# Optimization experiments

Hardware: AMD Instinct MI355X
Metric: run time of the kernel (lower is better)

## Reference

```python
import jax, jax.numpy as jnp
import numpy as np

D = 256        # d_model
B = 16
T = 8192
K = 100        # num_anchors
EPS = 1e-12    # normalize eps (matches torch sqrt(sum+eps))
LN_EPS = 1e-5  # nn.LayerNorm default
NEG = float(np.finfo(np.float32).min)


def _p(key, shape, scale=0.02):
    return (jax.random.normal(key, shape, dtype=jnp.float32) * scale)


def setup_inputs() -> dict:
    key = jax.random.key(0)
    ks = jax.random.split(key, 12)
    return {
        "vision_tokens": jax.random.normal(ks[0], (B, T, D), dtype=jnp.float32),
        "text_emb": jax.random.normal(ks[1], (B, D), dtype=jnp.float32),
        # fuse: Linear(2D->D), GELU, Linear(D->D)
        "fuse_w1": _p(ks[2], (2 * D, D)), "fuse_b1": jnp.zeros((D,), jnp.float32),
        "fuse_w2": _p(ks[3], (D, D)),     "fuse_b2": jnp.zeros((D,), jnp.float32),
        # box head: LN, Linear(D->D), GELU, Linear(D->4)
        "box_ln_g": jnp.ones((D,), jnp.float32), "box_ln_b": jnp.zeros((D,), jnp.float32),
        "box_w1": _p(ks[4], (D, D)), "box_b1": jnp.zeros((D,), jnp.float32),
        "box_w2": _p(ks[5], (D, 4)), "box_b2": jnp.zeros((4,), jnp.float32),
        # obj head: LN, Linear(D->D), GELU, Linear(D->1)
        "obj_ln_g": jnp.ones((D,), jnp.float32), "obj_ln_b": jnp.zeros((D,), jnp.float32),
        "obj_w1": _p(ks[6], (D, D)), "obj_b1": jnp.zeros((D,), jnp.float32),
        "obj_w2": _p(ks[7], (D, 1)), "obj_b2": jnp.zeros((1,), jnp.float32),
    }


def _layer_norm(x, g, b):
    mu = jnp.mean(x, axis=-1, keepdims=True)
    var = jnp.mean(jnp.square(x - mu), axis=-1, keepdims=True)
    return (x - mu) * jax.lax.rsqrt(var + LN_EPS) * g + b


def _gelu(x):
    return jax.nn.gelu(x, approximate=False)  # torch nn.GELU default is exact erf


def reference(vision_tokens, text_emb,
              fuse_w1, fuse_b1, fuse_w2, fuse_b2,
              box_ln_g, box_ln_b, box_w1, box_b1, box_w2, box_b2,
              obj_ln_g, obj_ln_b, obj_w1, obj_b1, obj_w2, obj_b2):
    # L2-normalize text embedding (sqrt(sum+eps) variant)
    txt = text_emb / jnp.sqrt(jnp.sum(text_emb * text_emb, axis=-1, keepdims=True) + EPS)  # (B,D)
    # broadcast-concat text to every token and fuse
    txt_b = jnp.broadcast_to(txt[:, None, :], vision_tokens.shape)  # (B,T,D)
    cat = jnp.concatenate([vision_tokens, txt_b], axis=-1)          # (B,T,2D)
    h = _gelu(cat @ fuse_w1 + fuse_b1) @ fuse_w2 + fuse_b2          # (B,T,D)
    # box head -> sigmoid xywh
    bh = _layer_norm(h, box_ln_g, box_ln_b)
    boxes = jax.nn.sigmoid(_gelu(bh @ box_w1 + box_b1) @ box_w2 + box_b2)  # (B,T,4)
    # objectness head -> sigmoid score per token
    oh = _layer_norm(h, obj_ln_g, obj_ln_b)
    obj = jax.nn.sigmoid(_gelu(oh @ obj_w1 + obj_b1) @ obj_w2 + obj_b2)[..., 0]  # (B,T)
    # pad with -inf-like min so topk always has K candidates, then clamp idx to T-1
    pad = jnp.full((obj.shape[0], K), NEG, dtype=obj.dtype)
    obj_pad = jnp.concatenate([obj, pad], axis=1)                   # (B,T+K)
    scores, idx_raw = jax.lax.top_k(obj_pad, K)                     # (B,K)
    idx = jnp.minimum(idx_raw, obj.shape[1] - 1)                    # (B,K)
    top_boxes = jnp.take_along_axis(boxes, idx[..., None], axis=1)  # (B,K,4)
    # cosine similarity of fused tokens vs. text
    tok_n = h / jnp.sqrt(jnp.sum(h * h, axis=-1, keepdims=True) + EPS)
    text_scores_full = jnp.sum(tok_n * txt[:, None, :], axis=-1)    # (B,T)
    top_text_scores = jnp.take_along_axis(text_scores_full, idx, axis=1)  # (B,K)
    return (top_boxes, scores, top_text_scores)
```

## Files before the change

### kernel.cpp

```cpp
#include <hip/hip_runtime.h>
#include <math.h>

#define D 256
#define PD 260
#define TOK_B 16
#define TOK_T 8192
#define NTOK (TOK_B * TOK_T)
#define KSEL 100

typedef unsigned long long ull;

__device__ float g_txt[TOK_B * D];
__device__ float g_obj[NTOK];
__device__ int   g_sel[TOK_B * KSEL];

template <typename F>
__device__ __forceinline__ float np_sum128_f(F f, int base) {
#pragma clang fp contract(off)
  float r0 = f(base + 0), r1 = f(base + 1), r2 = f(base + 2), r3 = f(base + 3);
  float r4 = f(base + 4), r5 = f(base + 5), r6 = f(base + 6), r7 = f(base + 7);
  for (int i = 8; i < 128; i += 8) {
    r0 += f(base + i + 0); r1 += f(base + i + 1);
    r2 += f(base + i + 2); r3 += f(base + i + 3);
    r4 += f(base + i + 4); r5 += f(base + i + 5);
    r6 += f(base + i + 6); r7 += f(base + i + 7);
  }
  return ((r0 + r1) + (r2 + r3)) + ((r4 + r5) + (r6 + r7));
}
template <typename F>
__device__ __forceinline__ float np_sum256_f(F f) {
#pragma clang fp contract(off)
  return np_sum128_f(f, 0) + np_sum128_f(f, 128);
}

template <typename F>
__device__ __forceinline__ float np_sum256_par8(F f, int j) {
#pragma clang fp contract(off)
  float s0 = f(j);
  for (int i = 1; i < 16; ++i) s0 += f(8 * i + j);
  float s1 = f(128 + j);
  for (int i = 1; i < 16; ++i) s1 += f(128 + 8 * i + j);
  s0 += __shfl_xor(s0, 1);
  s0 += __shfl_xor(s0, 2);
  s0 += __shfl_xor(s0, 4);
  s1 += __shfl_xor(s1, 1);
  s1 += __shfl_xor(s1, 2);
  s1 += __shfl_xor(s1, 4);
  return s0 + s1;
}

__device__ __forceinline__ float np_geluf(float x) {
#pragma clang fp contract(off)
  const float t = x / 1.41421356237309504880f;
  const float e = (float)erf((double)t);
  return (0.5f * x) * (1.0f + e);
}
__device__ __forceinline__ float np_sigmoidf(float x) {
#pragma clang fp contract(off)
  return 1.0f / (1.0f + expf(-x));
}

__global__ __launch_bounds__(256) void k0_txt(const float* __restrict__ text_emb) {
#pragma clang fp contract(off)
  const int b = blockIdx.x, tid = threadIdx.x;
  __shared__ float sSq[D];
  __shared__ float sTot;
  const float e = text_emb[b * D + tid];
  sSq[tid] = e * e;
  __syncthreads();
  if (tid == 0) {
    const float* p = sSq;
    sTot = np_sum256_f([&](int i) { return p[i]; });
  }
  __syncthreads();
  g_txt[b * D + tid] = e / sqrtf(sTot + 1e-12f);
}

__device__ __forceinline__ void gemm_acc(const float (*__restrict__ S)[PD],
                                         const float* __restrict__ W, int r0,
                                         int c0, float acc[4][8]) {
  for (int k = 0; k < D; k += 4) {
    float4 A0 = *(const float4*)&S[r0 + 0][k];
    float4 A1 = *(const float4*)&S[r0 + 1][k];
    float4 A2 = *(const float4*)&S[r0 + 2][k];
    float4 A3 = *(const float4*)&S[r0 + 3][k];
    const float ar[4][4] = {{A0.x, A0.y, A0.z, A0.w},
                            {A1.x, A1.y, A1.z, A1.w},
                            {A2.x, A2.y, A2.z, A2.w},
                            {A3.x, A3.y, A3.z, A3.w}};
#pragma unroll
    for (int kk = 0; kk < 4; ++kk) {
      const float* wr = W + (size_t)(k + kk) * D + c0;
      float4 W0 = *(const float4*)wr;
      float4 W1 = *(const float4*)(wr + 4);
      const float wv[8] = {W0.x, W0.y, W0.z, W0.w, W1.x, W1.y, W1.z, W1.w};
#pragma unroll
      for (int i = 0; i < 4; ++i)
#pragma unroll
        for (int j = 0; j < 8; ++j)
          acc[i][j] = fmaf(ar[i][kk], wv[j], acc[i][j]);
    }
  }
}

__global__ __launch_bounds__(256) void k1_obj(
    const float* __restrict__ vision, const float* __restrict__ fuse_w1,
    const float* __restrict__ fuse_b1, const float* __restrict__ fuse_w2,
    const float* __restrict__ fuse_b2, const float* __restrict__ obj_ln_g,
    const float* __restrict__ obj_ln_b, const float* __restrict__ obj_w1,
    const float* __restrict__ obj_b1, const float* __restrict__ obj_w2,
    const float* __restrict__ obj_b2) {
#pragma clang fp contract(off)
  const int tid = threadIdx.x;
  const int tr = tid >> 5, tc = tid & 31;
  const int r0 = tr << 2, c0 = tc << 3;
  const int blk = blockIdx.x;
  const int batch = blk >> 8;

  __shared__ float sA[32][PD];
  __shared__ float sTxt[D];
  __shared__ float sMu[32], sRstd[32];

  {
    const float* src = vision + (size_t)blk * (32 * D);
#pragma unroll
    for (int i = 0; i < 8; ++i) {
      const int e = i * 1024 + tid * 4;
      const int row = e >> 8, col = e & 255;
      *(float4*)&sA[row][col] = *(const float4*)(src + e);
    }
    sTxt[tid] = g_txt[batch * D + tid];
  }
  __syncthreads();

  float acc[4][8];
#pragma unroll
  for (int i = 0; i < 4; ++i)
#pragma unroll
    for (int j = 0; j < 8; ++j) acc[i][j] = 0.0f;

  gemm_acc(sA, fuse_w1, r0, c0, acc);
  for (int k = 0; k < D; ++k) {
    const float tv = sTxt[k];
    const float* wr = fuse_w1 + (size_t)(D + k) * D + c0;
    float4 W0 = *(const float4*)wr;
    float4 W1 = *(const float4*)(wr + 4);
    const float wv[8] = {W0.x, W0.y, W0.z, W0.w, W1.x, W1.y, W1.z, W1.w};
#pragma unroll
    for (int i = 0; i < 4; ++i)
#pragma unroll
      for (int j = 0; j < 8; ++j) acc[i][j] = fmaf(tv, wv[j], acc[i][j]);
  }
  __syncthreads();
  {
#pragma unroll
    for (int j2 = 0; j2 < 8; ++j2) {
      const float b = fuse_b1[c0 + j2];
#pragma unroll
      for (int i = 0; i < 4; ++i)
        sA[r0 + i][c0 + j2] = np_geluf(acc[i][j2] + b);
    }
  }
  __syncthreads();

#pragma unroll
  for (int i = 0; i < 4; ++i)
#pragma unroll
    for (int j = 0; j < 8; ++j) acc[i][j] = 0.0f;
  gemm_acc(sA, fuse_w2, r0, c0, acc);
  __syncthreads();
  {
#pragma unroll
    for (int j2 = 0; j2 < 8; ++j2) {
      const float b = fuse_b2[c0 + j2];
#pragma unroll
      for (int i = 0; i < 4; ++i) sA[r0 + i][c0 + j2] = acc[i][j2] + b;
    }
  }
  __syncthreads();

  {
    const int r = tid >> 3, j = tid & 7;
    const float* hrow = &sA[r][0];
    const float mu =
        np_sum256_par8([&](int i) { return hrow[i]; }, j) / 256.0f;
    const float var = np_sum256_par8(
                          [&](int i) {
                            const float d = hrow[i] - mu;
                            return d * d;
                          },
                          j) /
                      256.0f;
    if (j == 0) {
      sMu[r] = mu;
      sRstd[r] = 1.0f / sqrtf(var + 1e-5f);
    }
  }
  __syncthreads();

  {
    const float lg = obj_ln_g[tid], lb = obj_ln_b[tid];
    for (int r = 0; r < 32; ++r) {
      const float t = (sA[r][tid] - sMu[r]) * sRstd[r];
      sA[r][tid] = t * lg + lb;
    }
  }
  __syncthreads();

#pragma unroll
  for (int i = 0; i < 4; ++i)
#pragma unroll
    for (int j = 0; j < 8; ++j) acc[i][j] = 0.0f;
  gemm_acc(sA, obj_w1, r0, c0, acc);
  __syncthreads();
  {
#pragma unroll
    for (int j2 = 0; j2 < 8; ++j2) {
      const float b = obj_b1[c0 + j2];
#pragma unroll
      for (int i = 0; i < 4; ++i)
        sA[r0 + i][c0 + j2] = np_geluf(acc[i][j2] + b);
    }
  }
  __syncthreads();

  if ((tid & 7) == 0) {
    const int row = tid >> 3;
    const float* q = &sA[row][0];
    float L = 0.0f;
    for (int k = 0; k < D; ++k) L = fmaf(q[k], obj_w2[k], L);
    L = L + obj_b2[0];
    g_obj[(size_t)blk * 32 + row] = np_sigmoidf(L);
  }
}

__global__ __launch_bounds__(256) void k2_topk(float* __restrict__ out_scores) {
  const int b = blockIdx.x, tid = threadIdx.x;
  __shared__ ull sKey[TOK_T];
  __shared__ ull sGmax[128];
  __shared__ int sWin;
  for (int i = tid; i < TOK_T; i += 256) {
    const float s = g_obj[b * TOK_T + i];
    sKey[i] = ((ull)__float_as_uint(s) << 32) | (unsigned)(TOK_T - 1 - i);
  }
  __syncthreads();
  if (tid < 128) {
    ull m = 0ull;
    for (int j = 0; j < 64; ++j) {
      const ull v = sKey[tid + 128 * j];
      m = v > m ? v : m;
    }
    sGmax[tid] = m;
  }
  __syncthreads();
  for (int r = 0; r < KSEL; ++r) {
    if (tid < 64) {
      ull m = sGmax[tid];
      const ull o = sGmax[64 + tid];
      if (o > m) m = o;
#pragma unroll
      for (int off = 32; off > 0; off >>= 1) {
        const ull o2 = __shfl_down(m, off, 64);
        if (o2 > m) m = o2;
      }
      if (tid == 0) {
        const int idx = (TOK_T - 1) - (int)(unsigned)(m & 0xFFFFFFFFull);
        out_scores[b * KSEL + r] = __uint_as_float((unsigned)(m >> 32));
        g_sel[b * KSEL + r] = idx;
        sKey[idx] = 0ull;
        sWin = idx & 127;
      }
    }
    __syncthreads();
    if (tid < 64) {
      const int g = sWin;
      ull v = sKey[g + 128 * tid];
#pragma unroll
      for (int off = 32; off > 0; off >>= 1) {
        const ull o = __shfl_down(v, off, 64);
        if (o > v) v = o;
      }
      if (tid == 0) sGmax[g] = v;
    }
    __syncthreads();
  }
}

__global__ __launch_bounds__(256) void k3_box(
    const float* __restrict__ vision, const float* __restrict__ fuse_w1,
    const float* __restrict__ fuse_b1, const float* __restrict__ fuse_w2,
    const float* __restrict__ fuse_b2, const float* __restrict__ box_ln_g,
    const float* __restrict__ box_ln_b, const float* __restrict__ box_w1,
    const float* __restrict__ box_b1, const float* __restrict__ box_w2,
    const float* __restrict__ box_b2, float* __restrict__ out) {
#pragma clang fp contract(off)
  const int tid = threadIdx.x, c = tid;
  __shared__ float sV[8][PD];
  __shared__ float sG[8][PD];
  __shared__ float sH[8][PD];
  __shared__ float sTx[8][PD];
  __shared__ float sMu[8], sRstd[8];
  __shared__ int sIdx[8], sBat[8];
  if (tid < 8) {
    const int e = blockIdx.x * 8 + tid;
    sBat[tid] = e / KSEL;
    sIdx[tid] = g_sel[e];
  }
  __syncthreads();
  {
    const int u = tid >> 5, col = (tid & 31) * 8;
    const float* src = vision + ((size_t)sBat[u] * TOK_T + sIdx[u]) * D + col;
    *(float4*)&sV[u][col] = *(const float4*)src;
    *(float4*)&sV[u][col + 4] = *(const float4*)(src + 4);
    const float* tsrc = &g_txt[sBat[u] * D + col];
    *(float4*)&sTx[u][col] = *(const float4*)tsrc;
    *(float4*)&sTx[u][col + 4] = *(const float4*)(tsrc + 4);
  }
  __syncthreads();

  float acc[8];
#pragma unroll
  for (int u = 0; u < 8; ++u) acc[u] = 0.0f;
  for (int k = 0; k < D; ++k) {
    const float w = fuse_w1[k * D + c];
#pragma unroll
    for (int u = 0; u < 8; ++u) acc[u] = fmaf(sV[u][k], w, acc[u]);
  }
  for (int k = 0; k < D; ++k) {
    const float w = fuse_w1[(D + k) * D + c];
#pragma unroll
    for (int u = 0; u < 8; ++u) acc[u] = fmaf(sTx[u][k], w, acc[u]);
  }
  {
    const float b = fuse_b1[c];
#pragma unroll
    for (int u = 0; u < 8; ++u) sG[u][c] = np_geluf(acc[u] + b);
  }
  __syncthreads();

#pragma unroll
  for (int u = 0; u < 8; ++u) acc[u] = 0.0f;
  for (int k = 0; k < D; ++k) {
    const float w = fuse_w2[k * D + c];
#pragma unroll
    for (int u = 0; u < 8; ++u) acc[u] = fmaf(sG[u][k], w, acc[u]);
  }
  {
    const float b = fuse_b2[c];
#pragma unroll
    for (int u = 0; u < 8; ++u) sH[u][c] = acc[u] + b;
  }
  __syncthreads();

  {
    const int u = tid >> 3, j = tid & 7;
    if (u < 8) {
      const float* h = &sH[u][0];
      const float* tx = &sTx[u][0];
      const float mu = np_sum256_par8([&](int i) { return h[i]; }, j) / 256.0f;
      const float var = np_sum256_par8(
                            [&](int i) {
                              const float d = h[i] - mu;
                              return d * d;
                            },
                            j) /
                        256.0f;
      const float q2 = np_sum256_par8([&](int i) { return h[i] * h[i]; }, j);
      const float den = sqrtf(q2 + 1e-12f);
      const float ts =
          np_sum256_par8([&](int i) { return (h[i] / den) * tx[i]; }, j);
      if (j == 0) {
        sMu[u] = mu;
        sRstd[u] = 1.0f / sqrtf(var + 1e-5f);
        out[8000 + blockIdx.x * 8 + u] = ts;
      }
    }
  }
  __syncthreads();

  {
    const float lg = box_ln_g[c], lb = box_ln_b[c];
#pragma unroll
    for (int u = 0; u < 8; ++u) {
      const float t = (sH[u][c] - sMu[u]) * sRstd[u];
      sG[u][c] = t * lg + lb;
    }
  }
  __syncthreads();

#pragma unroll
  for (int u = 0; u < 8; ++u) acc[u] = 0.0f;
  for (int k = 0; k < D; ++k) {
    const float w = box_w1[k * D + c];
#pragma unroll
    for (int u = 0; u < 8; ++u) acc[u] = fmaf(sG[u][k], w, acc[u]);
  }
  {
    const float b = box_b1[c];
#pragma unroll
    for (int u = 0; u < 8; ++u) sV[u][c] = np_geluf(acc[u] + b);
  }
  __syncthreads();

  if (tid < 32) {
    const int u = tid >> 2, j = tid & 3;
    const float* q = &sV[u][0];
    float L = 0.0f;
    for (int k = 0; k < D; ++k) L = fmaf(q[k], box_w2[k * 4 + j], L);
    L = L + box_b2[j];
    out[(blockIdx.x * 8 + u) * 4 + j] = np_sigmoidf(L);
  }
}

extern "C" void kernel_launch(void* const* d_in, const int* in_sizes, int n_in,
                              void* d_out, int out_size, void* d_ws,
                              size_t ws_size, hipStream_t stream) {
  const float* vision   = (const float*)d_in[0];
  const float* text_emb = (const float*)d_in[1];
  const float* fuse_w1  = (const float*)d_in[2];
  const float* fuse_b1  = (const float*)d_in[3];
  const float* fuse_w2  = (const float*)d_in[4];
  const float* fuse_b2  = (const float*)d_in[5];
  const float* box_ln_g = (const float*)d_in[6];
  const float* box_ln_b = (const float*)d_in[7];
  const float* box_w1   = (const float*)d_in[8];
  const float* box_b1   = (const float*)d_in[9];
  const float* box_w2   = (const float*)d_in[10];
  const float* box_b2   = (const float*)d_in[11];
  const float* obj_ln_g = (const float*)d_in[12];
  const float* obj_ln_b = (const float*)d_in[13];
  const float* obj_w1   = (const float*)d_in[14];
  const float* obj_b1   = (const float*)d_in[15];
  const float* obj_w2   = (const float*)d_in[16];
  const float* obj_b2   = (const float*)d_in[17];
  float* out = (float*)d_out;

  k0_txt<<<TOK_B, 256, 0, stream>>>(text_emb);
  k1_obj<<<NTOK / 32, 256, 0, stream>>>(
      vision, fuse_w1, fuse_b1, fuse_w2, fuse_b2, obj_ln_g, obj_ln_b, obj_w1,
      obj_b1, obj_w2, obj_b2);
  k2_topk<<<TOK_B, 256, 0, stream>>>(out + 6400);
  k3_box<<<(TOK_B * KSEL) / 8, 256, 0, stream>>>(
      vision, fuse_w1, fuse_b1, fuse_w2, fuse_b2, box_ln_g, box_ln_b, box_w1,
      box_b1, box_w2, box_b2, out);
}
```

Before: 1.404 ms.

## Stage weight tiles through LDS in k1_obj GEMMs instead of direct global loads

The weight matrices in the fused obj-path kernel are now loaded cooperatively into a shared-memory tile of 32 k-rows per step, with a padded per-column-group layout. Each thread then reads its 8 output columns from LDS rather than issuing per-thread global float4 loads. Some barriers are folded into the tile loop, and launch bounds now request 2 blocks per SM. The aim is to cut redundant global/L2 weight traffic; the cost is extra LDS use (about 33 KB more per block), which may reduce occupancy, plus many more barriers.

```diff
diff --git a/kernel.cpp b/kernel.cpp
--- a/kernel.cpp
+++ b/kernel.cpp
@@ -3,10 +3,12 @@
 
 #define D 256
 #define PD 260
+#define SWS 260
 #define TOK_B 16
 #define TOK_T 8192
 #define NTOK (TOK_B * TOK_T)
 #define KSEL 100
+#define ROWS 32
 
 typedef unsigned long long ull;
 
@@ -76,34 +78,86 @@
   g_txt[b * D + tid] = e / sqrtf(sTot + 1e-12f);
 }
 
-__device__ __forceinline__ void gemm_acc(const float (*__restrict__ S)[PD],
-                                         const float* __restrict__ W, int r0,
-                                         int c0, float acc[4][8]) {
-  for (int k = 0; k < D; k += 4) {
-    float4 A0 = *(const float4*)&S[r0 + 0][k];
-    float4 A1 = *(const float4*)&S[r0 + 1][k];
-    float4 A2 = *(const float4*)&S[r0 + 2][k];
-    float4 A3 = *(const float4*)&S[r0 + 3][k];
-    const float ar[4][4] = {{A0.x, A0.y, A0.z, A0.w},
-                            {A1.x, A1.y, A1.z, A1.w},
-                            {A2.x, A2.y, A2.z, A2.w},
-                            {A3.x, A3.y, A3.z, A3.w}};
-#pragma unroll
-    for (int kk = 0; kk < 4; ++kk) {
-      const float* wr = W + (size_t)(k + kk) * D + c0;
-      float4 W0 = *(const float4*)wr;
-      float4 W1 = *(const float4*)(wr + 4);
+__device__ __forceinline__ void gemm_lds(const float (*__restrict__ S)[PD],
+                                         const float* __restrict__ W,
+                                         float* __restrict__ sW, int r0,
+                                         int tc, float acc[4][8]) {
+  const int t = threadIdx.x;
+  const int sg = t & 31, kb = t >> 5;
+  for (int kt = 0; kt < 8; ++kt) {
+    __syncthreads();
+#pragma unroll
+    for (int m = 0; m < 4; ++m) {
+      const int k = kb * 4 + m;
+      const float* src = W + (size_t)(kt * 32 + k) * D + sg * 8;
+      const float4 a = *(const float4*)src;
+      const float4 b = *(const float4*)(src + 4);
+      float* dst = sW + sg * SWS + k * 8;
+      *(float4*)dst = a;
+      *(float4*)(dst + 4) = b;
+    }
+    __syncthreads();
+    const float* wp = sW + tc * SWS;
+    const int kbase = kt * 32;
+    for (int k4 = 0; k4 < 32; k4 += 4) {
+      const float4 A0 = *(const float4*)&S[r0 + 0][kbase + k4];
+      const float4 A1 = *(const float4*)&S[r0 + 1][kbase + k4];
+      const float4 A2 = *(const float4*)&S[r0 + 2][kbase + k4];
+      const float4 A3 = *(const float4*)&S[r0 + 3][kbase + k4];
+      const float ar[4][4] = {{A0.x, A0.y, A0.z, A0.w},
+                              {A1.x, A1.y, A1.z, A1.w},
+                              {A2.x, A2.y, A2.z, A2.w},
+                              {A3.x, A3.y, A3.z, A3.w}};
+#pragma unroll
+      for (int kk = 0; kk < 4; ++kk) {
+        const float4 W0 = *(const float4*)(wp + (k4 + kk) * 8);
+        const float4 W1 = *(const float4*)(wp + (k4 + kk) * 8 + 4);
+        const float wv[8] = {W0.x, W0.y, W0.z, W0.w, W1.x, W1.y, W1.z, W1.w};
+#pragma unroll
+        for (int i = 0; i < 4; ++i)
+#pragma unroll
+          for (int j = 0; j < 8; ++j)
+            acc[i][j] = fmaf(ar[i][kk], wv[j], acc[i][j]);
+      }
+    }
+  }
+}
+
+__device__ __forceinline__ void gemm_txt_lds(const float* __restrict__ sTxt,
+                                             const float* __restrict__ W,
+                                             float* __restrict__ sW, int tc,
+                                             float acc[4][8]) {
+  const int t = threadIdx.x;
+  const int sg = t & 31, kb = t >> 5;
+  for (int kt = 0; kt < 8; ++kt) {
+    __syncthreads();
+#pragma unroll
+    for (int m = 0; m < 4; ++m) {
+      const int k = kb * 4 + m;
+      const float* src = W + (size_t)(kt * 32 + k) * D + sg * 8;
+      const float4 a = *(const float4*)src;
+      const float4 b = *(const float4*)(src + 4);
+      float* dst = sW + sg * SWS + k * 8;
+      *(float4*)dst = a;
+      *(float4*)(dst + 4) = b;
+    }
+    __syncthreads();
+    const float* wp = sW + tc * SWS;
+    const int kbase = kt * 32;
+    for (int k = 0; k < 32; ++k) {
+      const float tv = sTxt[kbase + k];
+      const float4 W0 = *(const float4*)(wp + k * 8);
+      const float4 W1 = *(const float4*)(wp + k * 8 + 4);
       const float wv[8] = {W0.x, W0.y, W0.z, W0.w, W1.x, W1.y, W1.z, W1.w};
 #pragma unroll
       for (int i = 0; i < 4; ++i)
 #pragma unroll
-        for (int j = 0; j < 8; ++j)
-          acc[i][j] = fmaf(ar[i][kk], wv[j], acc[i][j]);
-    }
-  }
-}
-
-__global__ __launch_bounds__(256) void k1_obj(
+        for (int j = 0; j < 8; ++j) acc[i][j] = fmaf(tv, wv[j], acc[i][j]);
+    }
+  }
+}
+
+__global__ __launch_bounds__(256, 2) void k1_obj(
     const float* __restrict__ vision, const float* __restrict__ fuse_w1,
     const float* __restrict__ fuse_b1, const float* __restrict__ fuse_w2,
     const float* __restrict__ fuse_b2, const float* __restrict__ obj_ln_g,
@@ -117,12 +171,13 @@
   const int blk = blockIdx.x;
   const int batch = blk >> 8;
 
-  __shared__ float sA[32][PD];
+  __shared__ float sA[ROWS][PD];
+  __shared__ float sW[32 * SWS];
   __shared__ float sTxt[D];
-  __shared__ float sMu[32], sRstd[32];
-
-  {
-    const float* src = vision + (size_t)blk * (32 * D);
+  __shared__ float sMu[ROWS], sRstd[ROWS];
+
+  {
+    const float* src = vision + (size_t)blk * (ROWS * D);
 #pragma unroll
     for (int i = 0; i < 8; ++i) {
       const int e = i * 1024 + tid * 4;
@@ -131,7 +186,6 @@
     }
     sTxt[tid] = g_txt[batch * D + tid];
   }
-  __syncthreads();
 
   float acc[4][8];
 #pragma unroll
@@ -139,18 +193,8 @@
 #pragma unroll
     for (int j = 0; j < 8; ++j) acc[i][j] = 0.0f;
 
-  gemm_acc(sA, fuse_w1, r0, c0, acc);
-  for (int k = 0; k < D; ++k) {
-    const float tv = sTxt[k];
-    const float* wr = fuse_w1 + (size_t)(D + k) * D + c0;
-    float4 W0 = *(const float4*)wr;
-    float4 W1 = *(const float4*)(wr + 4);
-    const float wv[8] = {W0.x, W0.y, W0.z, W0.w, W1.x, W1.y, W1.z, W1.w};
-#pragma unroll
-    for (int i = 0; i < 4; ++i)
-#pragma unroll
-      for (int j = 0; j < 8; ++j) acc[i][j] = fmaf(tv, wv[j], acc[i][j]);
-  }
+  gemm_lds(sA, fuse_w1, sW, r0, tc, acc);
+  gemm_txt_lds(sTxt, fuse_w1 + (size_t)D * D, sW, tc, acc);
   __syncthreads();
   {
 #pragma unroll
@@ -161,13 +205,12 @@
         sA[r0 + i][c0 + j2] = np_geluf(acc[i][j2] + b);
     }
   }
-  __syncthreads();
 
 #pragma unroll
   for (int i = 0; i < 4; ++i)
 #pragma unroll
     for (int j = 0; j < 8; ++j) acc[i][j] = 0.0f;
-  gemm_acc(sA, fuse_w2, r0, c0, acc);
+  gemm_lds(sA, fuse_w2, sW, r0, tc, acc);
   __syncthreads();
   {
 #pragma unroll
@@ -200,18 +243,17 @@
 
   {
     const float lg = obj_ln_g[tid], lb = obj_ln_b[tid];
-    for (int r = 0; r < 32; ++r) {
+    for (int r = 0; r < ROWS; ++r) {
       const float t = (sA[r][tid] - sMu[r]) * sRstd[r];
       sA[r][tid] = t * lg + lb;
     }
   }
-  __syncthreads();
 
 #pragma unroll
   for (int i = 0; i < 4; ++i)
 #pragma unroll
     for (int j = 0; j < 8; ++j) acc[i][j] = 0.0f;
-  gemm_acc(sA, obj_w1, r0, c0, acc);
+  gemm_lds(sA, obj_w1, sW, r0, tc, acc);
   __syncthreads();
   {
 #pragma unroll
@@ -230,7 +272,7 @@
     float L = 0.0f;
     for (int k = 0; k < D; ++k) L = fmaf(q[k], obj_w2[k], L);
     L = L + obj_b2[0];
-    g_obj[(size_t)blk * 32 + row] = np_sigmoidf(L);
+    g_obj[(size_t)blk * ROWS + row] = np_sigmoidf(L);
   }
 }
 
@@ -436,7 +478,7 @@
   float* out = (float*)d_out;
 
   k0_txt<<<TOK_B, 256, 0, stream>>>(text_emb);
-  k1_obj<<<NTOK / 32, 256, 0, stream>>>(
+  k1_obj<<<NTOK / ROWS, 256, 0, stream>>>(
       vision, fuse_w1, fuse_b1, fuse_w2, fuse_b2, obj_ln_g, obj_ln_b, obj_w1,
       obj_b1, obj_w2, obj_b2);
   k2_topk<<<TOK_B, 256, 0, stream>>>(out + 6400);
```

Measured after the change: 1.484 ms. +5.7%, slower.
